# Optimization experiments

Hardware: AMD Instinct MI355X
Metric: run time of the kernel (lower is better)

The kernel has to match this reference:

```python
import jax, jax.numpy as jnp
import numpy as np

N, L, H, E = 4, 2048, 8, 64
S, D = 2048, 64
EPS = 1e-6

def setup_inputs() -> dict:
    key = jax.random.key(0)
    k1, k2, k3 = jax.random.split(key, 3)
    return {
        "queries": jax.random.normal(k1, (N, L, H, E), dtype=jnp.float32),
        "keys": jax.random.normal(k2, (N, S, H, E), dtype=jnp.float32),
        "values": jax.random.normal(k3, (N, S, H, D), dtype=jnp.float32),
        "key_mask": jnp.ones((N, S), dtype=jnp.float32),
    }

def reference(queries, keys, values, key_mask):
    n, l, h, e = queries.shape
    _, s, _, d = values.shape
    softmax_temp = 1.0 / np.sqrt(e).astype(np.float32)
    # Faithful to torch: .view(N,H,L,E) is a reshape of the contiguous
    # (N,L,H,E) buffer, NOT a transpose.
    q = queries.reshape(n, h, l, e)
    k = keys.reshape(n, h, s, e)
    # squared euclidean distance ||q_i - k_j||^2 via expansion (== cdist^2)
    q_sq = jnp.sum(q * q, axis=-1)  # [n,h,l]
    k_sq = jnp.sum(k * k, axis=-1)  # [n,h,s]
    qk = jnp.einsum('nhle,nhse->nhls', q, k)
    dist_sq = jnp.maximum(q_sq[..., :, None] + k_sq[..., None, :] - 2.0 * qk, 0.0)
    phi = jnp.exp(-softmax_temp * (dist_sq * 0.5))  # [n,h,l,s]
    phi = phi * key_mask[:, None, None, :]
    Z = 1.0 / (jnp.sum(phi, axis=-1) + EPS)  # [n,h,l]
    out = jnp.einsum('nhls,nshd,nhl->nlhd', phi, values, Z)
    return out
```

## Files before the change

### kernel.cpp

```cpp
#include <hip/hip_runtime.h>
#include <stdint.h>


#define N_ 4
#define L_ 2048
#define H_ 8
#define S_ 2048

#define C1 0.18033688f
#define C2 0.09016844f

typedef unsigned short ushort_t;
typedef unsigned int uint_t;
typedef __bf16 b8 __attribute__((ext_vector_type(8)));
typedef float f4 __attribute__((ext_vector_type(4)));
typedef const __attribute__((address_space(1))) uint32_t* gas_ptr;
typedef __attribute__((address_space(3))) uint32_t* las_ptr;

static __device__ __forceinline__ ushort_t f2bf(float x) {
  uint32_t u = __float_as_uint(x);
  u += 0x7fffu + ((u >> 16) & 1u);
  return (ushort_t)(u >> 16);
}

__global__ __launch_bounds__(256) void k_cvtk(const float* __restrict__ src,
                                              ushort_t* __restrict__ dst,
                                              float* __restrict__ lbf,
                                              const float* __restrict__ mask) {
  int t = blockIdx.x * 256 + threadIdx.x;
  int row = t >> 2, part = t & 3;
  const float4* p = reinterpret_cast<const float4*>(src + (size_t)row * 64 + part * 16);
  uint_t o[8];
  float s = 0.f;
#pragma unroll
  for (int i = 0; i < 4; ++i) {
    float4 v = p[i];
    s += v.x * v.x + v.y * v.y + v.z * v.z + v.w * v.w;
    o[2 * i]     = (uint_t)f2bf(v.x) | ((uint_t)f2bf(v.y) << 16);
    o[2 * i + 1] = (uint_t)f2bf(v.z) | ((uint_t)f2bf(v.w) << 16);
  }
  uint4* dp = reinterpret_cast<uint4*>(dst + (size_t)row * 64 + part * 16);
  dp[0] = make_uint4(o[0], o[1], o[2], o[3]);
  dp[1] = make_uint4(o[4], o[5], o[6], o[7]);
  s += __shfl_xor(s, 1);
  s += __shfl_xor(s, 2);
  if (part == 0) {
    int n = row >> 14;
    int sidx = row & (S_ - 1);
    float m = mask[n * S_ + sidx];
    lbf[row] = -C2 * s + __log2f(m);
  }
}

__global__ __launch_bounds__(256) void k_vt(const float* __restrict__ v,
                                            ushort_t* __restrict__ vt) {
  __shared__ __align__(16) ushort_t tile[64][68];
  const int n = blockIdx.z, h = blockIdx.y, sc = blockIdx.x;
  const int t = threadIdx.x;
  const int sl = t >> 4;
  const int dp = (t & 15) * 4;
#pragma unroll
  for (int i = 0; i < 4; ++i) {
    int s = sc * 64 + i * 16 + sl;
    float4 val = *reinterpret_cast<const float4*>(
        v + (((size_t)n * S_ + s) * H_ + h) * 64 + dp);
    tile[dp + 0][i * 16 + sl] = f2bf(val.x);
    tile[dp + 1][i * 16 + sl] = f2bf(val.y);
    tile[dp + 2][i * 16 + sl] = f2bf(val.z);
    tile[dp + 3][i * 16 + sl] = f2bf(val.w);
  }
  __syncthreads();
  const int d = t >> 2, sp = (t & 3) * 16;
  uint_t o[8];
#pragma unroll
  for (int i = 0; i < 8; ++i) {
    const int p0 = sp + 2 * i, p1 = p0 + 1;
    const int s0 = (p0 & 32) + (((p0 >> 2) & 1) << 4) + (((p0 >> 3) & 3) << 2) + (p0 & 3);
    const int s1 = (p1 & 32) + (((p1 >> 2) & 1) << 4) + (((p1 >> 3) & 3) << 2) + (p1 & 3);
    o[i] = (uint_t)tile[d][s0] | ((uint_t)tile[d][s1] << 16);
  }
  size_t base = ((size_t)(n * H_ + h) * 64 + d) * S_ + sc * 64 + sp;
  uint4* w = reinterpret_cast<uint4*>(vt + base);
  w[0] = make_uint4(o[0], o[1], o[2], o[3]);
  w[1] = make_uint4(o[4], o[5], o[6], o[7]);
}

__global__ __launch_bounds__(256, 4) void k_attn(
    const float* __restrict__ qf32, const ushort_t* __restrict__ kb,
    const ushort_t* __restrict__ vt, const float* __restrict__ lbf,
    float* __restrict__ out) {
  __shared__ __align__(16) ushort_t kt[2][64 * 64];
  __shared__ __align__(16) ushort_t vtt[2][64 * 64];
  __shared__ __align__(16) float zb[4][16];

  const int lane = threadIdx.x & 63;
  const int w = threadIdx.x >> 6;
  const int bid = blockIdx.x;
  const int swz = (bid & 7) * 128 + (bid >> 3);
  const int qt = swz & 31;
  const int hd = (swz >> 5) & 7;
  const int n = swz >> 8;
  const int nh = n * H_ + hd;
  const int c = lane & 15;
  const int g = lane >> 4;
  const int qrow0 = qt * 64 + w * 16;

  union U4 { uint_t u[4]; b8 v; };

  const float* qsrc = qf32 + ((size_t)nh * L_ + qrow0) * 64;
  b8 qfr[2];
  float epsr;
  {
    const float* rp = qsrc + (size_t)c * 64 + g * 8;
    float s = 0.f;
#pragma unroll
    for (int es = 0; es < 2; ++es) {
      float4 v0 = *reinterpret_cast<const float4*>(rp + es * 32);
      float4 v1 = *reinterpret_cast<const float4*>(rp + es * 32 + 4);
      s += v0.x * v0.x + v0.y * v0.y + v0.z * v0.z + v0.w * v0.w
         + v1.x * v1.x + v1.y * v1.y + v1.z * v1.z + v1.w * v1.w;
      U4 tq;
      tq.u[0] = (uint_t)f2bf(v0.x) | ((uint_t)f2bf(v0.y) << 16);
      tq.u[1] = (uint_t)f2bf(v0.z) | ((uint_t)f2bf(v0.w) << 16);
      tq.u[2] = (uint_t)f2bf(v1.x) | ((uint_t)f2bf(v1.y) << 16);
      tq.u[3] = (uint_t)f2bf(v1.z) | ((uint_t)f2bf(v1.w) << 16);
      qfr[es] = tq.v;
    }
    s += __shfl_xor(s, 16);
    s += __shfl_xor(s, 32);
    epsr = 1e-6f * exp2f(C2 * s);
  }

  const ushort_t* kbh = kb + (size_t)nh * S_ * 64;
  const ushort_t* vth = vt + (size_t)nh * 64 * S_;
  const float* lbh = lbf + (size_t)nh * S_;

  f4 zero4 = {0.f, 0.f, 0.f, 0.f};
  f4 acc[4] = {zero4, zero4, zero4, zero4};
  float rs = 0.f;

  const int lrow = lane >> 3;
  const int lc16 = (lane & 7) ^ lrow;

  float4 lbA[4], lbB[4];

#define WAITV8 asm volatile("s_waitcnt vmcnt(8)" ::: "memory")
#define WAITV4 asm volatile("s_waitcnt vmcnt(4)" ::: "memory")

#define STAGE(bufi, ch)                                                        \
  {                                                                            \
    _Pragma("unroll")                                                          \
    for (int t2 = 0; t2 < 2; ++t2) {                                           \
      const int rr = w * 16 + t2 * 8;                                          \
      const ushort_t* gk = kbh + ((size_t)(ch) * 64 + rr + lrow) * 64 + lc16 * 8; \
      __builtin_amdgcn_global_load_lds((gas_ptr)gk, (las_ptr)(&kt[bufi][rr * 64]), 16, 0, 0); \
      const ushort_t* gv = vth + (size_t)(rr + lrow) * S_ + (ch) * 64 + lc16 * 8; \
      __builtin_amdgcn_global_load_lds((gas_ptr)gv, (las_ptr)(&vtt[bufi][rr * 64]), 16, 0, 0); \
    }                                                                          \
  }

#define LBLOAD(dst, ch)                                                        \
  {                                                                            \
    _Pragma("unroll")                                                          \
    for (int ss = 0; ss < 4; ++ss)                                             \
      dst[ss] = *reinterpret_cast<const float4*>(lbh + (ch) * 64 + ss * 16 + 4 * g); \
  }

#define CHUNK(CH, BUF, LBC, LBN, DO_LB, DO_S, WAITX)                           \
  {                                                                            \
    WAITX;                                                                     \
    __builtin_amdgcn_s_barrier();                                              \
    __builtin_amdgcn_sched_barrier(0);                                         \
    uint_t pw[8];                                                              \
    _Pragma("unroll")                                                          \
    for (int ss = 0; ss < 4; ++ss) {                                           \
      const ushort_t* ktb = &kt[BUF][(ss * 16 + c) * 64];                      \
      b8 ak0 = *reinterpret_cast<const b8*>(ktb + (g ^ (c & 7)) * 8);          \
      b8 ak1 = *reinterpret_cast<const b8*>(ktb + ((4 + g) ^ (c & 7)) * 8);    \
      __builtin_amdgcn_s_setprio(1);                                           \
      f4 s0 = __builtin_amdgcn_mfma_f32_16x16x32_bf16(ak0, qfr[0], zero4, 0, 0, 0); \
      s0 = __builtin_amdgcn_mfma_f32_16x16x32_bf16(ak1, qfr[1], s0, 0, 0, 0);  \
      __builtin_amdgcn_s_setprio(0);                                           \
      float p0 = exp2f(fmaf(C1, s0[0], LBC[ss].x));                            \
      float p1 = exp2f(fmaf(C1, s0[1], LBC[ss].y));                            \
      float p2 = exp2f(fmaf(C1, s0[2], LBC[ss].z));                            \
      float p3 = exp2f(fmaf(C1, s0[3], LBC[ss].w));                            \
      rs += (p0 + p1) + (p2 + p3);                                             \
      asm("v_cvt_pk_bf16_f32 %0, %1, %2" : "=v"(pw[2 * ss])     : "v"(p0), "v"(p1)); \
      asm("v_cvt_pk_bf16_f32 %0, %1, %2" : "=v"(pw[2 * ss + 1]) : "v"(p2), "v"(p3)); \
    }                                                                          \
    __builtin_amdgcn_s_setprio(1);                                             \
    _Pragma("unroll")                                                          \
    for (int sst = 0; sst < 2; ++sst) {                                        \
      U4 pa;                                                                   \
      pa.u[0] = pw[4 * sst + 0]; pa.u[1] = pw[4 * sst + 1];                    \
      pa.u[2] = pw[4 * sst + 2]; pa.u[3] = pw[4 * sst + 3];                    \
      _Pragma("unroll")                                                        \
      for (int db = 0; db < 4; ++db) {                                         \
        b8 bv = *reinterpret_cast<const b8*>(                                  \
            &vtt[BUF][(db * 16 + c) * 64] + (((4 * sst + g) ^ (c & 7)) * 8));  \
        acc[db] = __builtin_amdgcn_mfma_f32_16x16x32_bf16(pa.v, bv, acc[db], 0, 0, 0); \
      }                                                                        \
    }                                                                          \
    __builtin_amdgcn_s_setprio(0);                                             \
    __builtin_amdgcn_sched_barrier(0);                                         \
    __builtin_amdgcn_s_barrier();                                              \
    if (DO_LB) { LBLOAD(LBN, (CH) + 1); }                                      \
    __builtin_amdgcn_sched_barrier(0);                                         \
    if (DO_S) { STAGE(BUF, (CH) + 2); }                                        \
  }

  STAGE(0, 0);
  LBLOAD(lbA, 0);
  __builtin_amdgcn_sched_barrier(0);
  STAGE(1, 1);

  for (int ch = 0; ch < 28; ch += 2) {
    CHUNK(ch,     0, lbA, lbB, true, true, WAITV8);
    CHUNK(ch + 1, 1, lbB, lbA, true, true, WAITV8);
  }
  CHUNK(28, 0, lbA, lbB, true,  true,  WAITV8);
  CHUNK(29, 1, lbB, lbA, true,  true,  WAITV8);
  CHUNK(30, 0, lbA, lbB, true,  false, WAITV8);
  CHUNK(31, 1, lbB, lbA, false, false, WAITV4);

#undef CHUNK
#undef STAGE
#undef LBLOAD
#undef WAITV8
#undef WAITV4

  rs += __shfl_xor(rs, 16);
  rs += __shfl_xor(rs, 32);
  if (g == 0) zb[w][c] = 1.f / (rs + epsr);
  __syncthreads();

  const float4 z4 = *reinterpret_cast<const float4*>(&zb[w][4 * g]);
  const float zz[4] = {z4.x, z4.y, z4.z, z4.w};
  float* ob = out + (((size_t)n * L_ + qrow0 + 4 * g) * H_ + hd) * 64;
#pragma unroll
  for (int db = 0; db < 4; ++db) {
#pragma unroll
    for (int r = 0; r < 4; ++r) {
      ob[(size_t)r * (H_ * 64) + db * 16 + c] = acc[db][r] * zz[r];
    }
  }
}

extern "C" void kernel_launch(void* const* d_in, const int* in_sizes, int n_in,
                              void* d_out, int out_size, void* d_ws, size_t ws_size,
                              hipStream_t stream) {
  const float* q = (const float*)d_in[0];
  const float* k = (const float*)d_in[1];
  const float* v = (const float*)d_in[2];
  const float* mask = (const float*)d_in[3];
  float* out = (float*)d_out;

  char* ws = (char*)d_ws;
  ushort_t* kb = (ushort_t*)ws;
  ushort_t* vt = (ushort_t*)(ws + ((size_t)8 << 20));
  float* lbf = (float*)(ws + ((size_t)16 << 20));

  k_cvtk<<<dim3(1024), dim3(256), 0, stream>>>(k, kb, lbf, mask);
  k_vt<<<dim3(S_ / 64, H_, N_), dim3(256), 0, stream>>>(v, vt);
  k_attn<<<dim3(1024), dim3(256), 0, stream>>>(q, kb, vt, lbf, out);
}
```

Measured before the change: 81.26 us.

## Process two query sub-tiles per wave to reuse staged K/V tiles

Each wave now handles 32 query rows instead of 16, so every K and V fragment read from LDS feeds two MFMAs. The grid shrinks from 1024 to 512 blocks and the launch bound drops to 2 blocks per SM. LDS addresses are precomputed per lane with a buffer offset, and the chunk loop is no longer unrolled. The aim is to halve global and LDS traffic for K/V per query row, at the cost of higher register use, lower occupancy and fewer blocks to spread over the CUs.

```diff
diff --git a/kernel.cpp b/kernel.cpp
--- a/kernel.cpp
+++ b/kernel.cpp
@@ -85,33 +85,34 @@
   w[1] = make_uint4(o[4], o[5], o[6], o[7]);
 }
 
-__global__ __launch_bounds__(256, 4) void k_attn(
+__global__ __launch_bounds__(256, 2) void k_attn(
     const float* __restrict__ qf32, const ushort_t* __restrict__ kb,
     const ushort_t* __restrict__ vt, const float* __restrict__ lbf,
     float* __restrict__ out) {
   __shared__ __align__(16) ushort_t kt[2][64 * 64];
   __shared__ __align__(16) ushort_t vtt[2][64 * 64];
-  __shared__ __align__(16) float zb[4][16];
+  __shared__ __align__(16) float zb[4][32];
 
   const int lane = threadIdx.x & 63;
   const int w = threadIdx.x >> 6;
   const int bid = blockIdx.x;
-  const int swz = (bid & 7) * 128 + (bid >> 3);
-  const int qt = swz & 31;
-  const int hd = (swz >> 5) & 7;
-  const int n = swz >> 8;
+  const int swz = (bid & 7) * 64 + (bid >> 3);
+  const int qt = swz & 15;
+  const int hd = (swz >> 4) & 7;
+  const int n = swz >> 7;
   const int nh = n * H_ + hd;
   const int c = lane & 15;
   const int g = lane >> 4;
-  const int qrow0 = qt * 64 + w * 16;
+  const int qrow0 = qt * 128 + w * 32;
 
   union U4 { uint_t u[4]; b8 v; };
 
   const float* qsrc = qf32 + ((size_t)nh * L_ + qrow0) * 64;
-  b8 qfr[2];
-  float epsr;
-  {
-    const float* rp = qsrc + (size_t)c * 64 + g * 8;
+  b8 qfr0[2], qfr1[2];
+  float epsr[2];
+#pragma unroll
+  for (int qb2 = 0; qb2 < 2; ++qb2) {
+    const float* rp = qsrc + (size_t)(qb2 * 16 + c) * 64 + g * 8;
     float s = 0.f;
 #pragma unroll
     for (int es = 0; es < 2; ++es) {
@@ -124,11 +125,11 @@
       tq.u[1] = (uint_t)f2bf(v0.z) | ((uint_t)f2bf(v0.w) << 16);
       tq.u[2] = (uint_t)f2bf(v1.x) | ((uint_t)f2bf(v1.y) << 16);
       tq.u[3] = (uint_t)f2bf(v1.z) | ((uint_t)f2bf(v1.w) << 16);
-      qfr[es] = tq.v;
+      if (qb2 == 0) qfr0[es] = tq.v; else qfr1[es] = tq.v;
     }
     s += __shfl_xor(s, 16);
     s += __shfl_xor(s, 32);
-    epsr = 1e-6f * exp2f(C2 * s);
+    epsr[qb2] = 1e-6f * exp2f(C2 * s);
   }
 
   const ushort_t* kbh = kb + (size_t)nh * S_ * 64;
@@ -136,8 +137,22 @@
   const float* lbh = lbf + (size_t)nh * S_;
 
   f4 zero4 = {0.f, 0.f, 0.f, 0.f};
-  f4 acc[4] = {zero4, zero4, zero4, zero4};
-  float rs = 0.f;
+  f4 acc0[4] = {zero4, zero4, zero4, zero4};
+  f4 acc1[4] = {zero4, zero4, zero4, zero4};
+  float rs0 = 0.f, rs1 = 0.f;
+
+  const ushort_t* kA[8];
+  const ushort_t* vA[8];
+#pragma unroll
+  for (int ss = 0; ss < 4; ++ss) {
+    kA[2 * ss]     = &kt[0][(ss * 16 + c) * 64 + (g ^ (c & 7)) * 8];
+    kA[2 * ss + 1] = &kt[0][(ss * 16 + c) * 64 + ((4 + g) ^ (c & 7)) * 8];
+  }
+#pragma unroll
+  for (int sst = 0; sst < 2; ++sst)
+#pragma unroll
+    for (int db = 0; db < 4; ++db)
+      vA[4 * sst + db] = &vtt[0][(db * 16 + c) * 64 + (((4 * sst + g) ^ (c & 7)) * 8)];
 
   const int lrow = lane >> 3;
   const int lc16 = (lane & 7) ^ lrow;
@@ -147,15 +162,15 @@
 #define WAITV8 asm volatile("s_waitcnt vmcnt(8)" ::: "memory")
 #define WAITV4 asm volatile("s_waitcnt vmcnt(4)" ::: "memory")
 
-#define STAGE(bufi, ch)                                                        \
+#define STAGE(BOFF, ch)                                                        \
   {                                                                            \
     _Pragma("unroll")                                                          \
     for (int t2 = 0; t2 < 2; ++t2) {                                           \
       const int rr = w * 16 + t2 * 8;                                          \
       const ushort_t* gk = kbh + ((size_t)(ch) * 64 + rr + lrow) * 64 + lc16 * 8; \
-      __builtin_amdgcn_global_load_lds((gas_ptr)gk, (las_ptr)(&kt[bufi][rr * 64]), 16, 0, 0); \
+      __builtin_amdgcn_global_load_lds((gas_ptr)gk, (las_ptr)(&kt[0][rr * 64] + (BOFF)), 16, 0, 0); \
       const ushort_t* gv = vth + (size_t)(rr + lrow) * S_ + (ch) * 64 + lc16 * 8; \
-      __builtin_amdgcn_global_load_lds((gas_ptr)gv, (las_ptr)(&vtt[bufi][rr * 64]), 16, 0, 0); \
+      __builtin_amdgcn_global_load_lds((gas_ptr)gv, (las_ptr)(&vtt[0][rr * 64] + (BOFF)), 16, 0, 0); \
     }                                                                          \
   }
 
@@ -166,40 +181,50 @@
       dst[ss] = *reinterpret_cast<const float4*>(lbh + (ch) * 64 + ss * 16 + 4 * g); \
   }
 
-#define CHUNK(CH, BUF, LBC, LBN, DO_LB, DO_S, WAITX)                           \
+#define CHUNK(CH, BOFF, LBC, LBN, DO_LB, DO_S, WAITX)                          \
   {                                                                            \
     WAITX;                                                                     \
     __builtin_amdgcn_s_barrier();                                              \
     __builtin_amdgcn_sched_barrier(0);                                         \
-    uint_t pw[8];                                                              \
+    uint_t pw0[8], pw1[8];                                                     \
     _Pragma("unroll")                                                          \
     for (int ss = 0; ss < 4; ++ss) {                                           \
-      const ushort_t* ktb = &kt[BUF][(ss * 16 + c) * 64];                      \
-      b8 ak0 = *reinterpret_cast<const b8*>(ktb + (g ^ (c & 7)) * 8);          \
-      b8 ak1 = *reinterpret_cast<const b8*>(ktb + ((4 + g) ^ (c & 7)) * 8);    \
+      b8 ak0 = *reinterpret_cast<const b8*>(kA[2 * ss] + (BOFF));              \
+      b8 ak1 = *reinterpret_cast<const b8*>(kA[2 * ss + 1] + (BOFF));          \
       __builtin_amdgcn_s_setprio(1);                                           \
-      f4 s0 = __builtin_amdgcn_mfma_f32_16x16x32_bf16(ak0, qfr[0], zero4, 0, 0, 0); \
-      s0 = __builtin_amdgcn_mfma_f32_16x16x32_bf16(ak1, qfr[1], s0, 0, 0, 0);  \
+      f4 s0 = __builtin_amdgcn_mfma_f32_16x16x32_bf16(ak0, qfr0[0], zero4, 0, 0, 0); \
+      s0 = __builtin_amdgcn_mfma_f32_16x16x32_bf16(ak1, qfr0[1], s0, 0, 0, 0); \
+      f4 s1 = __builtin_amdgcn_mfma_f32_16x16x32_bf16(ak0, qfr1[0], zero4, 0, 0, 0); \
+      s1 = __builtin_amdgcn_mfma_f32_16x16x32_bf16(ak1, qfr1[1], s1, 0, 0, 0); \
       __builtin_amdgcn_s_setprio(0);                                           \
-      float p0 = exp2f(fmaf(C1, s0[0], LBC[ss].x));                            \
-      float p1 = exp2f(fmaf(C1, s0[1], LBC[ss].y));                            \
-      float p2 = exp2f(fmaf(C1, s0[2], LBC[ss].z));                            \
-      float p3 = exp2f(fmaf(C1, s0[3], LBC[ss].w));                            \
-      rs += (p0 + p1) + (p2 + p3);                                             \
-      asm("v_cvt_pk_bf16_f32 %0, %1, %2" : "=v"(pw[2 * ss])     : "v"(p0), "v"(p1)); \
-      asm("v_cvt_pk_bf16_f32 %0, %1, %2" : "=v"(pw[2 * ss + 1]) : "v"(p2), "v"(p3)); \
+      float p00 = exp2f(fmaf(C1, s0[0], LBC[ss].x));                           \
+      float p01 = exp2f(fmaf(C1, s0[1], LBC[ss].y));                           \
+      float p02 = exp2f(fmaf(C1, s0[2], LBC[ss].z));                           \
+      float p03 = exp2f(fmaf(C1, s0[3], LBC[ss].w));                           \
+      float p10 = exp2f(fmaf(C1, s1[0], LBC[ss].x));                           \
+      float p11 = exp2f(fmaf(C1, s1[1], LBC[ss].y));                           \
+      float p12 = exp2f(fmaf(C1, s1[2], LBC[ss].z));                           \
+      float p13 = exp2f(fmaf(C1, s1[3], LBC[ss].w));                           \
+      rs0 += (p00 + p01) + (p02 + p03);                                        \
+      rs1 += (p10 + p11) + (p12 + p13);                                        \
+      asm("v_cvt_pk_bf16_f32 %0, %1, %2" : "=v"(pw0[2 * ss])     : "v"(p00), "v"(p01)); \
+      asm("v_cvt_pk_bf16_f32 %0, %1, %2" : "=v"(pw0[2 * ss + 1]) : "v"(p02), "v"(p03)); \
+      asm("v_cvt_pk_bf16_f32 %0, %1, %2" : "=v"(pw1[2 * ss])     : "v"(p10), "v"(p11)); \
+      asm("v_cvt_pk_bf16_f32 %0, %1, %2" : "=v"(pw1[2 * ss + 1]) : "v"(p12), "v"(p13)); \
     }                                                                          \
     __builtin_amdgcn_s_setprio(1);                                             \
     _Pragma("unroll")                                                          \
     for (int sst = 0; sst < 2; ++sst) {                                        \
-      U4 pa;                                                                   \
-      pa.u[0] = pw[4 * sst + 0]; pa.u[1] = pw[4 * sst + 1];                    \
-      pa.u[2] = pw[4 * sst + 2]; pa.u[3] = pw[4 * sst + 3];                    \
+      U4 pa0, pa1;                                                             \
+      pa0.u[0] = pw0[4 * sst + 0]; pa0.u[1] = pw0[4 * sst + 1];                \
+      pa0.u[2] = pw0[4 * sst + 2]; pa0.u[3] = pw0[4 * sst + 3];                \
+      pa1.u[0] = pw1[4 * sst + 0]; pa1.u[1] = pw1[4 * sst + 1];                \
+      pa1.u[2] = pw1[4 * sst + 2]; pa1.u[3] = pw1[4 * sst + 3];                \
       _Pragma("unroll")                                                        \
       for (int db = 0; db < 4; ++db) {                                         \
-        b8 bv = *reinterpret_cast<const b8*>(                                  \
-            &vtt[BUF][(db * 16 + c) * 64] + (((4 * sst + g) ^ (c & 7)) * 8));  \
-        acc[db] = __builtin_amdgcn_mfma_f32_16x16x32_bf16(pa.v, bv, acc[db], 0, 0, 0); \
+        b8 bv = *reinterpret_cast<const b8*>(vA[4 * sst + db] + (BOFF));       \
+        acc0[db] = __builtin_amdgcn_mfma_f32_16x16x32_bf16(pa0.v, bv, acc0[db], 0, 0, 0); \
+        acc1[db] = __builtin_amdgcn_mfma_f32_16x16x32_bf16(pa1.v, bv, acc1[db], 0, 0, 0); \
       }                                                                        \
     }                                                                          \
     __builtin_amdgcn_s_setprio(0);                                             \
@@ -207,22 +232,21 @@
     __builtin_amdgcn_s_barrier();                                              \
     if (DO_LB) { LBLOAD(LBN, (CH) + 1); }                                      \
     __builtin_amdgcn_sched_barrier(0);                                         \
-    if (DO_S) { STAGE(BUF, (CH) + 2); }                                        \
+    if (DO_S) { STAGE(BOFF, (CH) + 2); }                                       \
   }
 
   STAGE(0, 0);
   LBLOAD(lbA, 0);
   __builtin_amdgcn_sched_barrier(0);
-  STAGE(1, 1);
-
-  for (int ch = 0; ch < 28; ch += 2) {
-    CHUNK(ch,     0, lbA, lbB, true, true, WAITV8);
-    CHUNK(ch + 1, 1, lbB, lbA, true, true, WAITV8);
-  }
-  CHUNK(28, 0, lbA, lbB, true,  true,  WAITV8);
-  CHUNK(29, 1, lbB, lbA, true,  true,  WAITV8);
-  CHUNK(30, 0, lbA, lbB, true,  false, WAITV8);
-  CHUNK(31, 1, lbB, lbA, false, false, WAITV4);
+  STAGE(4096, 1);
+
+#pragma unroll 1
+  for (int ch = 0; ch < 30; ch += 2) {
+    CHUNK(ch,     0,    lbA, lbB, true, true, WAITV8);
+    CHUNK(ch + 1, 4096, lbB, lbA, true, true, WAITV8);
+  }
+  CHUNK(30, 0,    lbA, lbB, true,  false, WAITV8);
+  CHUNK(31, 4096, lbB, lbA, false, false, WAITV4);
 
 #undef CHUNK
 #undef STAGE
@@ -230,19 +254,28 @@
 #undef WAITV8
 #undef WAITV4
 
-  rs += __shfl_xor(rs, 16);
-  rs += __shfl_xor(rs, 32);
-  if (g == 0) zb[w][c] = 1.f / (rs + epsr);
+  rs0 += __shfl_xor(rs0, 16);
+  rs0 += __shfl_xor(rs0, 32);
+  rs1 += __shfl_xor(rs1, 16);
+  rs1 += __shfl_xor(rs1, 32);
+  if (g == 0) {
+    zb[w][c]      = 1.f / (rs0 + epsr[0]);
+    zb[w][16 + c] = 1.f / (rs1 + epsr[1]);
+  }
   __syncthreads();
 
-  const float4 z4 = *reinterpret_cast<const float4*>(&zb[w][4 * g]);
-  const float zz[4] = {z4.x, z4.y, z4.z, z4.w};
-  float* ob = out + (((size_t)n * L_ + qrow0 + 4 * g) * H_ + hd) * 64;
-#pragma unroll
-  for (int db = 0; db < 4; ++db) {
-#pragma unroll
-    for (int r = 0; r < 4; ++r) {
-      ob[(size_t)r * (H_ * 64) + db * 16 + c] = acc[db][r] * zz[r];
+#pragma unroll
+  for (int qb2 = 0; qb2 < 2; ++qb2) {
+    const float4 z4 = *reinterpret_cast<const float4*>(&zb[w][qb2 * 16 + 4 * g]);
+    const float zz[4] = {z4.x, z4.y, z4.z, z4.w};
+    float* ob = out + (((size_t)n * L_ + qrow0 + qb2 * 16 + 4 * g) * H_ + hd) * 64;
+#pragma unroll
+    for (int db = 0; db < 4; ++db) {
+      const f4 a = qb2 ? acc1[db] : acc0[db];
+#pragma unroll
+      for (int r = 0; r < 4; ++r) {
+        ob[(size_t)r * (H_ * 64) + db * 16 + c] = a[r] * zz[r];
+      }
     }
   }
 }
@@ -263,5 +296,5 @@
 
   k_cvtk<<<dim3(1024), dim3(256), 0, stream>>>(k, kb, lbf, mask);
   k_vt<<<dim3(S_ / 64, H_, N_), dim3(256), 0, stream>>>(v, vt);
-  k_attn<<<dim3(1024), dim3(256), 0, stream>>>(q, kb, vt, lbf, out);
-}
+  k_attn<<<dim3(512), dim3(256), 0, stream>>>(q, kb, vt, lbf, out);
+}
```

Result: slower. 83.86 us (+3.2%).
